# Optimization experiments

Measured on AMD Instinct MI355X. Metric: run time of the kernel, lower is better.

The kernel has to match this reference:

```python
import jax, jax.numpy as jnp
import numpy as np

B, S, D = 2, 2048, 4096
H, ROT = 16, 64
HD = D // H  # 256


def rotate_every_two(x):
    # x: (..., d) with d even; interleave (-x_odd, x_even)
    x1 = x[..., ::2]
    x2 = x[..., 1::2]
    return jnp.stack((-x2, x1), axis=-1).reshape(x.shape)


def setup_inputs() -> dict:
    key = jax.random.key(0)
    ks = jax.random.split(key, 8)
    hidden_states = jax.random.normal(ks[0], (B, S, D), dtype=jnp.float32)
    # GPT-J style repeat-interleaved sin/cos over rotary_dim, broadcast over heads
    inv_freq = 1.0 / (10000.0 ** (jnp.arange(0, ROT, 2, dtype=jnp.float32) / ROT))
    t = jnp.arange(S, dtype=jnp.float32)
    freqs = jnp.einsum('s,f->sf', t, inv_freq)                    # (S, ROT/2)
    freqs = jnp.repeat(freqs, 2, axis=-1)                         # (S, ROT)
    sin = jnp.sin(freqs)[None, :, None, :]                        # (1, S, 1, ROT)
    cos = jnp.cos(freqs)[None, :, None, :]
    scale = 0.02
    Wq = jax.random.normal(ks[1], (D, D), dtype=jnp.float32) * scale
    Wk = jax.random.normal(ks[2], (D, D), dtype=jnp.float32) * scale
    Wv = jax.random.normal(ks[3], (D, D), dtype=jnp.float32) * scale
    Wo = jax.random.normal(ks[4], (D, D), dtype=jnp.float32) * scale
    return {"hidden_states": hidden_states, "sin": sin, "cos": cos,
            "Wq": Wq, "Wk": Wk, "Wv": Wv, "Wo": Wo}


def reference(hidden_states, sin, cos, Wq, Wk, Wv, Wo):
    b, s, d = hidden_states.shape
    # projections (nn.Linear, no bias): y = x @ W.T
    q = (hidden_states @ Wq.T).reshape(b, s, H, HD)
    k = (hidden_states @ Wk.T).reshape(b, s, H, HD)
    v = (hidden_states @ Wv.T).reshape(b, s, H, HD)

    def rope(x):
        x_rot, x_pass = x[..., :ROT], x[..., ROT:]
        x_rot = x_rot * cos + rotate_every_two(x_rot) * sin
        return jnp.concatenate([x_rot, x_pass], axis=-1)

    q = rope(q).transpose(0, 2, 1, 3)  # (B, H, S, HD)
    k = rope(k).transpose(0, 2, 1, 3)
    v = v.transpose(0, 2, 1, 3)

    inv_scale = 1.0 / np.sqrt(HD).astype(np.float32)
    scores = jnp.einsum('bhqd,bhkd->bhqk', q, k) * inv_scale      # (B, H, S, S)
    # scaled_masked_triangular_softmax == causal masked softmax
    causal = jnp.tril(jnp.ones((s, s), dtype=bool))
    scores = jnp.where(causal[None, None], scores, jnp.finfo(scores.dtype).min)
    attn = jax.nn.softmax(scores, axis=-1)
    out = jnp.einsum('bhqk,bhkd->bhqd', attn, v)                  # (B, H, S, HD)
    out = out.transpose(0, 2, 1, 3).reshape(b, s, d)              # merge heads
    return out @ Wo.T
```

## Files before the change

kernel.cpp:

```cpp
#include <hip/hip_runtime.h>
#include <cstdint>
#include <cstddef>

#define TB 2
#define TS 2048
#define TD 4096
#define TH 16
#define THD 256
#define TROT 64
#define TM (TB*TS)

typedef __attribute__((ext_vector_type(8))) short bf16x8;
typedef __attribute__((ext_vector_type(4))) float f32x4;

#define LGKM0  asm volatile("s_waitcnt lgkmcnt(0)" ::: "memory")
#define VMCNT8 asm volatile("s_waitcnt vmcnt(8)" ::: "memory")
#define VMCNT4 asm volatile("s_waitcnt vmcnt(4)" ::: "memory")
#define VMCNT0 asm volatile("s_waitcnt vmcnt(0)" ::: "memory")
#define SBAR   __builtin_amdgcn_s_barrier()
#define SCHED0 __builtin_amdgcn_sched_barrier(0)

__device__ __forceinline__ unsigned short f2bf(float f) {
  union { float f; unsigned u; } v; v.f = f;
  return (unsigned short)((v.u + 0x7fffu + ((v.u >> 16) & 1u)) >> 16);
}

__device__ __forceinline__ void gld16(const void* g, void* l) {
  __builtin_amdgcn_global_load_lds(
      (const __attribute__((address_space(1))) unsigned int*)g,
      (__attribute__((address_space(3))) unsigned int*)l, 16, 0, 0);
}

__global__ __launch_bounds__(256) void k_cvt5(
    const float* __restrict__ s0, const float* __restrict__ s1,
    const float* __restrict__ s2, const float* __restrict__ s3,
    const float* __restrict__ s4, unsigned short* __restrict__ dst) {
  int i = blockIdx.x * 256 + threadIdx.x;
  int tsel = i >> 22, il = i & 4194303;
  const float* s = tsel == 0 ? s0 : tsel == 1 ? s1 : tsel == 2 ? s2 : tsel == 3 ? s3 : s4;
  float4 v = reinterpret_cast<const float4*>(s)[il];
  ushort4 o;
  o.x = f2bf(v.x); o.y = f2bf(v.y); o.z = f2bf(v.z); o.w = f2bf(v.w);
  *reinterpret_cast<ushort4*>(dst + (size_t)i * 4) = o;
}

template<int MODE>
__global__ __launch_bounds__(512, 1) void k_gemm(
    const unsigned short* __restrict__ A, const unsigned short* __restrict__ W,
    void* __restrict__ out, const float* __restrict__ sinp, const float* __restrict__ cosp)
{
  extern __shared__ unsigned short lds[];
  const int K = TD;
  const int t = threadIdx.x;
  const int w = t >> 6, l = t & 63, lr = l & 15, lh = l >> 4;
  const int wm = w >> 2, wn = w & 3;

  const int id = blockIdx.x;
  const int swz = (id & 7) * 32 + (id >> 3);
  const int m0 = (swz >> 4) * 256, n0 = (swz & 15) * 256;

  const int llo = lr * 32 + ((lh ^ ((lr >> 1) & 3)) * 8);

  const unsigned short* srcA = A + (size_t)m0 * K;
  const unsigned short* srcB = W + (size_t)n0 * K;

  int roff[2];
#pragma unroll
  for (int it = 0; it < 2; ++it) {
    int c = it * 512 + t;
    int rl = (c >> 2) & 15;
    roff[it] = (16 * (c >> 7) + rl) * K + ((c >> 6) & 1) * 32 + ((c & 3) ^ ((rl >> 1) & 3)) * 8;
  }

  f32x4 acc[2][2][4][2];
#pragma unroll
  for (int qa = 0; qa < 2; ++qa)
#pragma unroll
    for (int qb = 0; qb < 2; ++qb)
#pragma unroll
      for (int m = 0; m < 4; ++m)
#pragma unroll
        for (int n = 0; n < 2; ++n) acc[qa][qb][m][n] = 0.f;

  bf16x8 af[4][2], bq0[2][2], bq1[2][2];

#define STG(SBUF, SAB, SHALF, SKOFS) { \
    const unsigned short* _s = (SAB) ? srcB : srcA; \
    const int _b = (SBUF)*32768 + (SAB)*16384 + (SHALF)*8192; \
    gld16(_s + (size_t)(SHALF)*128*TD + (SKOFS) + roff[0], &lds[_b + t*8]); \
    gld16(_s + (size_t)(SHALF)*128*TD + (SKOFS) + roff[1], &lds[_b + (512+t)*8]); }

#define PH(BUF, QA, QB, LDAF, LDB0, LDB1, SBUF, SAB, SHALF, SKOFS, DOVM) { \
    if (LDAF) { \
      _Pragma("unroll") for (int m = 0; m < 4; ++m) \
      _Pragma("unroll") for (int kk = 0; kk < 2; ++kk) \
        af[m][kk] = *(const bf16x8*)&lds[(BUF)*32768 + (QA)*8192 + ((wm*4+m)*2+kk)*512 + llo]; \
    } \
    if (LDB0) { \
      _Pragma("unroll") for (int n = 0; n < 2; ++n) \
      _Pragma("unroll") for (int kk = 0; kk < 2; ++kk) \
        bq0[n][kk] = *(const bf16x8*)&lds[(BUF)*32768 + 16384 + ((wn*2+n)*2+kk)*512 + llo]; \
    } \
    if (LDB1) { \
      _Pragma("unroll") for (int n = 0; n < 2; ++n) \
      _Pragma("unroll") for (int kk = 0; kk < 2; ++kk) \
        bq1[n][kk] = *(const bf16x8*)&lds[(BUF)*32768 + 16384 + 8192 + ((wn*2+n)*2+kk)*512 + llo]; \
    } \
    STG(SBUF, SAB, SHALF, SKOFS); \
    if (DOVM) { VMCNT4; } \
    SBAR; \
    if ((LDAF) || (LDB0) || (LDB1)) { LGKM0; } \
    SCHED0; \
    __builtin_amdgcn_s_setprio(1); \
    _Pragma("unroll") for (int kk = 0; kk < 2; ++kk) \
    _Pragma("unroll") for (int m = 0; m < 4; ++m) \
    _Pragma("unroll") for (int n = 0; n < 2; ++n) \
      acc[QA][QB][m][n] = __builtin_amdgcn_mfma_f32_16x16x32_bf16( \
          af[m][kk], (QB) ? bq1[n][kk] : bq0[n][kk], acc[QA][QB][m][n], 0,0,0); \
    __builtin_amdgcn_s_setprio(0); \
    SBAR; SCHED0; }

  const int NT = K / 64;

  STG(0,0,0, 0);  SCHED0;
  STG(0,1,0, 0);  SCHED0;
  STG(0,0,1, 0);  SCHED0;
  STG(0,1,1, 0);  SCHED0;
  STG(1,0,0, 64); SCHED0;
  STG(1,1,0, 64); SCHED0;
  VMCNT4; SBAR; SCHED0;

  for (int i2 = 0; i2 < NT/2; ++i2) {
    const int k1c = (2*i2+1) * 64;
    const int k0n = (2*i2+2 < NT ? 2*i2+2 : NT-1) * 64;
    const int k1n = (2*i2+3 < NT ? 2*i2+3 : NT-1) * 64;
    PH(0, 0,0, 1,1,0,  1,0,1, k1c, 0);
    PH(0, 0,1, 0,0,1,  1,1,1, k1c, 0);
    PH(0, 1,0, 1,0,0,  0,0,0, k0n, 0);
    PH(0, 1,1, 0,0,0,  0,1,0, k0n, 1);
    PH(1, 0,0, 1,1,0,  0,0,1, k0n, 0);
    PH(1, 0,1, 0,0,1,  0,1,1, k0n, 0);
    PH(1, 1,0, 1,0,0,  1,0,0, k1n, 0);
    PH(1, 1,1, 0,0,0,  1,1,0, k1n, 1);
  }
#undef PH
#undef STG

  VMCNT0;

  if constexpr (MODE == 2) {
    SBAR;
    const int b = m0 >> 11, sbase = m0 & (TS - 1);
#pragma unroll
    for (int qb = 0; qb < 2; ++qb)
#pragma unroll
      for (int n = 0; n < 2; ++n) {
        __syncthreads();
#pragma unroll
        for (int qa = 0; qa < 2; ++qa)
#pragma unroll
          for (int m = 0; m < 4; ++m) {
            int lcol = wn * 16 + lr;
            int srow = qa * 128 + wm * 64 + m * 16 + lh * 4;
            ushort4 o;
            o.x = f2bf(acc[qa][qb][m][n][0]); o.y = f2bf(acc[qa][qb][m][n][1]);
            o.z = f2bf(acc[qa][qb][m][n][2]); o.w = f2bf(acc[qa][qb][m][n][3]);
            *(ushort4*)&lds[lcol * 268 + srow] = o;
          }
        __syncthreads();
#pragma unroll
        for (int rr = 0; rr < 4; ++rr) {
          int idx = rr * 512 + t;
          int dl = idx >> 5, sc = (idx & 31) * 8;
          uint4 v = *(const uint4*)&lds[dl * 268 + sc];
          int d = n0 + qb * 128 + (dl >> 4) * 32 + n * 16 + (dl & 15);
          *(uint4*)((unsigned short*)out +
                    ((size_t)((b * TH + (d >> 8)) * THD + (d & 255))) * TS + sbase + sc) = v;
        }
      }
  } else {
#pragma unroll
    for (int qa = 0; qa < 2; ++qa)
#pragma unroll
      for (int qb = 0; qb < 2; ++qb)
#pragma unroll
        for (int m = 0; m < 4; ++m)
#pragma unroll
          for (int n = 0; n < 2; ++n)
#pragma unroll
            for (int r = 0; r < 4; ++r) {
              int row = m0 + qa * 128 + wm * 64 + m * 16 + lh * 4 + r;
              int col = n0 + qb * 128 + wn * 32 + n * 16 + lr;
              float x = acc[qa][qb][m][n][r];
              if constexpr (MODE == 0) {
                ((float*)out)[(size_t)row * TD + col] = x;
              } else {
                float part = __shfl_xor(x, 1, 64);
                int s = row & (TS - 1), b = row >> 11;
                int h = col >> 8, d = col & 255;
                float val = x;
                if (d < TROT) {
                  float cc = cosp[s * TROT + d], ss = sinp[s * TROT + d];
                  val = x * cc + ((d & 1) ? part : -part) * ss;
                }
                ((unsigned short*)out)[((size_t)(b * TH + h) * TS + s) * THD + d] = f2bf(val);
              }
            }
  }
}

__global__ __launch_bounds__(256, 2) void k_fattn(
    const unsigned short* __restrict__ Qt, const unsigned short* __restrict__ Kt,
    const unsigned short* __restrict__ Vt, unsigned short* __restrict__ O)
{
  extern __shared__ unsigned short sh[];
  const int t = threadIdx.x, w = t >> 6, l = t & 63, lr = l & 15, lh = l >> 4;
  const int bh = blockIdx.x;
  const int qb = (gridDim.y - 1) - blockIdx.y;
  const int q0 = qb * 64;
  const int jmax = qb;

  const unsigned short* kbase = Kt + (size_t)bh * TS * THD;
  const unsigned short* vbase = Vt + (size_t)bh * THD * TS;

  const int llo = lr * 32 + ((lh ^ ((lr >> 1) & 3)) * 8);

  int koff[8], voff[8];
#pragma unroll
  for (int it = 0; it < 8; ++it) {
    int c = it * 256 + t;
    int row = (c >> 2) & 15;
    int scc = (c & 3) ^ ((row >> 1) & 3);
    koff[it] = (((c >> 9) & 3) * 16 + row) * THD + ((c >> 6) & 7) * 32 + scc * 8;
    voff[it] = (((c >> 6) & 15) * 16 + row) * TS + ((c >> 10) & 1) * 32 + scc * 8;
  }

  bf16x8 qf[8];
  const unsigned short* qp = Qt + ((size_t)bh * TS + q0 + w * 16 + lr) * THD;
#pragma unroll
  for (int kk = 0; kk < 8; ++kk) qf[kk] = *(const bf16x8*)(qp + kk * 32 + lh * 8);

  f32x4 oacc[16];
#pragma unroll
  for (int i = 0; i < 16; ++i) oacc[i] = 0.f;
  float mrow[4] = {-__builtin_inff(), -__builtin_inff(), -__builtin_inff(), -__builtin_inff()};
  float lrow[4] = {0.f, 0.f, 0.f, 0.f};

#pragma unroll
  for (int it = 0; it < 8; ++it) gld16(kbase + koff[it], &sh[(it*256 + t) * 8]);
#pragma unroll
  for (int it = 0; it < 8; ++it) gld16(vbase + voff[it], &sh[16384 + (it*256 + t) * 8]);

  for (int j = 0; j <= jmax; ++j) {
    const bool nx = (j < jmax);
    VMCNT8; SBAR; SCHED0;

    f32x4 sacc[4];
#pragma unroll
    for (int nt = 0; nt < 4; ++nt) sacc[nt] = 0.f;
    __builtin_amdgcn_s_setprio(1);
#pragma unroll
    for (int kk = 0; kk < 8; ++kk)
#pragma unroll
      for (int nt = 0; nt < 4; ++nt) {
        bf16x8 kf = *(const bf16x8*)&sh[(nt*8 + kk)*512 + llo];
        sacc[nt] = __builtin_amdgcn_mfma_f32_16x16x32_bf16(qf[kk], kf, sacc[nt], 0, 0, 0);
      }
    __builtin_amdgcn_s_setprio(0);
    LGKM0; SBAR; SCHED0;
    if (nx) {
      const unsigned short* kj = kbase + (size_t)(j + 1) * 64 * THD;
#pragma unroll
      for (int it = 0; it < 8; ++it) gld16(kj + koff[it], &sh[(it*256 + t) * 8]);
    }

    float p[4][4], tmax[4];
    const int qrow0 = q0 + w * 16 + lh * 4;
#pragma unroll
    for (int r = 0; r < 4; ++r) tmax[r] = -__builtin_inff();
#pragma unroll
    for (int nt = 0; nt < 4; ++nt) {
      int kpos = j * 64 + nt * 16 + lr;
#pragma unroll
      for (int r = 0; r < 4; ++r) {
        float sv = sacc[nt][r] * 0.0625f;
        if (kpos > qrow0 + r) sv = -__builtin_inff();
        p[nt][r] = sv;
        tmax[r] = fmaxf(tmax[r], sv);
      }
    }
#pragma unroll
    for (int off = 1; off < 16; off <<= 1)
#pragma unroll
      for (int r = 0; r < 4; ++r) tmax[r] = fmaxf(tmax[r], __shfl_xor(tmax[r], off, 64));

    float g = fmaxf(fmaxf(tmax[0] - mrow[0], tmax[1] - mrow[1]),
                    fmaxf(tmax[2] - mrow[2], tmax[3] - mrow[3]));
    if (__any(g > 8.f)) {
      float alpha[4];
#pragma unroll
      for (int r = 0; r < 4; ++r) {
        float mn = fmaxf(mrow[r], tmax[r]);
        alpha[r] = __expf(mrow[r] - mn);
        mrow[r] = mn;
        lrow[r] *= alpha[r];
      }
#pragma unroll
      for (int i = 0; i < 16; ++i)
#pragma unroll
        for (int r = 0; r < 4; ++r) oacc[i][r] *= alpha[r];
    }

    float tsum[4] = {0.f, 0.f, 0.f, 0.f};
#pragma unroll
    for (int nt = 0; nt < 4; ++nt)
#pragma unroll
      for (int r = 0; r < 4; ++r) {
        float pe = __expf(p[nt][r] - mrow[r]);
        p[nt][r] = pe;
        tsum[r] += pe;
      }
#pragma unroll
    for (int off = 1; off < 16; off <<= 1)
#pragma unroll
      for (int r = 0; r < 4; ++r) tsum[r] += __shfl_xor(tsum[r], off, 64);
#pragma unroll
    for (int r = 0; r < 4; ++r) lrow[r] += tsum[r];

    const int wb = 32768 + w * 1152;
#pragma unroll
    for (int nt = 0; nt < 4; ++nt)
#pragma unroll
      for (int r = 0; r < 4; ++r)
        sh[wb + (lh*4 + r)*72 + nt*16 + lr] = f2bf(p[nt][r]);
    bf16x8 pfr0 = *(const bf16x8*)&sh[wb + lr*72 + lh*8];
    bf16x8 pfr1 = *(const bf16x8*)&sh[wb + lr*72 + 32 + lh*8];

    if (nx) { VMCNT8; } else { VMCNT0; }
    SBAR; SCHED0;
    __builtin_amdgcn_s_setprio(1);
#pragma unroll
    for (int dt = 0; dt < 16; ++dt) {
      bf16x8 vf = *(const bf16x8*)&sh[16384 + dt*512 + llo];
      oacc[dt] = __builtin_amdgcn_mfma_f32_16x16x32_bf16(pfr0, vf, oacc[dt], 0, 0, 0);
    }
#pragma unroll
    for (int dt = 0; dt < 16; ++dt) {
      bf16x8 vf = *(const bf16x8*)&sh[16384 + (16 + dt)*512 + llo];
      oacc[dt] = __builtin_amdgcn_mfma_f32_16x16x32_bf16(pfr1, vf, oacc[dt], 0, 0, 0);
    }
    __builtin_amdgcn_s_setprio(0);
    LGKM0; SBAR; SCHED0;
    if (nx) {
      const unsigned short* vj = vbase + (size_t)(j + 1) * 64;
#pragma unroll
      for (int it = 0; it < 8; ++it) gld16(vj + voff[it], &sh[16384 + (it*256 + t) * 8]);
    }
  }

  const int b = bh >> 4, h = bh & 15;
  float inv[4];
#pragma unroll
  for (int r = 0; r < 4; ++r) inv[r] = 1.f / lrow[r];
#pragma unroll
  for (int dt = 0; dt < 16; ++dt)
#pragma unroll
    for (int r = 0; r < 4; ++r) {
      int s = q0 + w * 16 + lh * 4 + r;
      O[((size_t)(b * TS + s) * TH + h) * THD + dt * 16 + lr] = f2bf(oacc[dt][r] * inv[r]);
    }
}

extern "C" void kernel_launch(void* const* d_in, const int* in_sizes, int n_in,
                              void* d_out, int out_size, void* d_ws, size_t ws_size,
                              hipStream_t stream) {
  const float* hs   = (const float*)d_in[0];
  const float* sinp = (const float*)d_in[1];
  const float* cosp = (const float*)d_in[2];
  const float* Wq   = (const float*)d_in[3];
  const float* Wk   = (const float*)d_in[4];
  const float* Wv   = (const float*)d_in[5];
  const float* Wo   = (const float*)d_in[6];

  const size_t NE = (size_t)TM * TD;
  const size_t BYTES = NE * 2;
  char* ws = (char*)d_ws;
  unsigned short* hsb = (unsigned short*)(ws + 0*BYTES);
  unsigned short* Wqb = (unsigned short*)(ws + 1*BYTES);
  unsigned short* Wkb = (unsigned short*)(ws + 2*BYTES);
  unsigned short* Wvb = (unsigned short*)(ws + 3*BYTES);
  unsigned short* Wob = (unsigned short*)(ws + 4*BYTES);
  unsigned short* Qt  = (unsigned short*)(ws + 5*BYTES);
  unsigned short* Ktb = (unsigned short*)(ws + 6*BYTES);
  unsigned short* Vtb = (unsigned short*)(ws + 7*BYTES);
  unsigned short* Ob  = (unsigned short*)(ws + 8*BYTES);

  k_cvt5<<<81920, 256, 0, stream>>>(hs, Wq, Wk, Wv, Wo, hsb);

  k_gemm<1><<<256, 512, 131072, stream>>>(hsb, Wqb, (void*)Qt,  sinp, cosp);
  k_gemm<1><<<256, 512, 131072, stream>>>(hsb, Wkb, (void*)Ktb, sinp, cosp);
  k_gemm<2><<<256, 512, 131072, stream>>>(hsb, Wvb, (void*)Vtb, nullptr, nullptr);

  k_fattn<<<dim3(TB*TH, TS/64), 256, 74752, stream>>>(Qt, Ktb, Vtb, Ob);

  k_gemm<0><<<256, 512, 131072, stream>>>(Ob, Wob, d_out, nullptr, nullptr);
}
```

Before: 725.0 us.

## Fuse QKV projections into one launch, rework GEMM phase loads, defer softmax reductions

The three Q/K/V projection GEMMs become a single 768-block launch over the concatenated weight buffers, selecting the Q, K or V epilogue from the output column tile. This removes two launches and the tail underutilisation of three 256-block grids. The GEMM main loop is restructured to prefetch the next LDS fragments inside the previous MFMA phase using double fragment registers. The flash-attention kernel drops the per-tile cross-lane max reduction unless a rescale is needed and defers the row-sum shuffle reduction to the end. The extra fragment registers raise register pressure, and the lazy max relies on a threshold of 8 for numerical safety.

```diff
diff --git a/kernel.cpp b/kernel.cpp
--- a/kernel.cpp
+++ b/kernel.cpp
@@ -19,6 +19,8 @@
 #define VMCNT0 asm volatile("s_waitcnt vmcnt(0)" ::: "memory")
 #define SBAR   __builtin_amdgcn_s_barrier()
 #define SCHED0 __builtin_amdgcn_sched_barrier(0)
+#define PRIO1  __builtin_amdgcn_s_setprio(1)
+#define PRIO0  __builtin_amdgcn_s_setprio(0)
 
 __device__ __forceinline__ unsigned short f2bf(float f) {
   union { float f; unsigned u; } v; v.f = f;
@@ -44,112 +46,126 @@
   *reinterpret_cast<ushort4*>(dst + (size_t)i * 4) = o;
 }
 
-template<int MODE>
-__global__ __launch_bounds__(512, 1) void k_gemm(
-    const unsigned short* __restrict__ A, const unsigned short* __restrict__ W,
-    void* __restrict__ out, const float* __restrict__ sinp, const float* __restrict__ cosp)
-{
-  extern __shared__ unsigned short lds[];
-  const int K = TD;
-  const int t = threadIdx.x;
-  const int w = t >> 6, l = t & 63, lr = l & 15, lh = l >> 4;
-  const int wm = w >> 2, wn = w & 3;
-
-  const int id = blockIdx.x;
-  const int swz = (id & 7) * 32 + (id >> 3);
-  const int m0 = (swz >> 4) * 256, n0 = (swz & 15) * 256;
-
-  const int llo = lr * 32 + ((lh ^ ((lr >> 1) & 3)) * 8);
-
-  const unsigned short* srcA = A + (size_t)m0 * K;
-  const unsigned short* srcB = W + (size_t)n0 * K;
-
-  int roff[2];
-#pragma unroll
-  for (int it = 0; it < 2; ++it) {
-    int c = it * 512 + t;
-    int rl = (c >> 2) & 15;
-    roff[it] = (16 * (c >> 7) + rl) * K + ((c >> 6) & 1) * 32 + ((c & 3) ^ ((rl >> 1) & 3)) * 8;
-  }
-
-  f32x4 acc[2][2][4][2];
-#pragma unroll
-  for (int qa = 0; qa < 2; ++qa)
-#pragma unroll
-    for (int qb = 0; qb < 2; ++qb)
-#pragma unroll
-      for (int m = 0; m < 4; ++m)
-#pragma unroll
-        for (int n = 0; n < 2; ++n) acc[qa][qb][m][n] = 0.f;
-
-  bf16x8 af[4][2], bq0[2][2], bq1[2][2];
-
-#define STG(SBUF, SAB, SHALF, SKOFS) { \
+#define GSTG(SBUF, SAB, SHALF, SKOFS) { \
     const unsigned short* _s = (SAB) ? srcB : srcA; \
     const int _b = (SBUF)*32768 + (SAB)*16384 + (SHALF)*8192; \
     gld16(_s + (size_t)(SHALF)*128*TD + (SKOFS) + roff[0], &lds[_b + t*8]); \
     gld16(_s + (size_t)(SHALF)*128*TD + (SKOFS) + roff[1], &lds[_b + (512+t)*8]); }
 
-#define PH(BUF, QA, QB, LDAF, LDB0, LDB1, SBUF, SAB, SHALF, SKOFS, DOVM) { \
-    if (LDAF) { \
-      _Pragma("unroll") for (int m = 0; m < 4; ++m) \
-      _Pragma("unroll") for (int kk = 0; kk < 2; ++kk) \
-        af[m][kk] = *(const bf16x8*)&lds[(BUF)*32768 + (QA)*8192 + ((wm*4+m)*2+kk)*512 + llo]; \
-    } \
-    if (LDB0) { \
-      _Pragma("unroll") for (int n = 0; n < 2; ++n) \
-      _Pragma("unroll") for (int kk = 0; kk < 2; ++kk) \
-        bq0[n][kk] = *(const bf16x8*)&lds[(BUF)*32768 + 16384 + ((wn*2+n)*2+kk)*512 + llo]; \
-    } \
-    if (LDB1) { \
-      _Pragma("unroll") for (int n = 0; n < 2; ++n) \
-      _Pragma("unroll") for (int kk = 0; kk < 2; ++kk) \
-        bq1[n][kk] = *(const bf16x8*)&lds[(BUF)*32768 + 16384 + 8192 + ((wn*2+n)*2+kk)*512 + llo]; \
-    } \
-    STG(SBUF, SAB, SHALF, SKOFS); \
-    if (DOVM) { VMCNT4; } \
-    SBAR; \
-    if ((LDAF) || (LDB0) || (LDB1)) { LGKM0; } \
-    SCHED0; \
-    __builtin_amdgcn_s_setprio(1); \
+#define GLD_AF(DST, BUF, QA) { \
+    _Pragma("unroll") for (int m = 0; m < 4; ++m) \
+    _Pragma("unroll") for (int kk = 0; kk < 2; ++kk) \
+      DST[m][kk] = *(const bf16x8*)&lds[(BUF)*32768 + (QA)*8192 + ((wm*4+m)*2+kk)*512 + llo]; }
+
+#define GLD_BQ(DST, BUF, QB) { \
+    _Pragma("unroll") for (int n = 0; n < 2; ++n) \
+    _Pragma("unroll") for (int kk = 0; kk < 2; ++kk) \
+      DST[n][kk] = *(const bf16x8*)&lds[(BUF)*32768 + 16384 + (QB)*8192 + ((wn*2+n)*2+kk)*512 + llo]; }
+
+#define GMF(AF, BQ, QA, QB) { \
     _Pragma("unroll") for (int kk = 0; kk < 2; ++kk) \
     _Pragma("unroll") for (int m = 0; m < 4; ++m) \
     _Pragma("unroll") for (int n = 0; n < 2; ++n) \
       acc[QA][QB][m][n] = __builtin_amdgcn_mfma_f32_16x16x32_bf16( \
-          af[m][kk], (QB) ? bq1[n][kk] : bq0[n][kk], acc[QA][QB][m][n], 0,0,0); \
-    __builtin_amdgcn_s_setprio(0); \
-    SBAR; SCHED0; }
-
+          AF[m][kk], BQ[n][kk], acc[QA][QB][m][n], 0,0,0); }
+
+#define GEMM_MAIN_LOOP \
+  GSTG(0,0,0, 0);  SCHED0; \
+  GSTG(0,1,0, 0);  SCHED0; \
+  GSTG(0,0,1, 0);  SCHED0; \
+  GSTG(0,1,1, 0);  SCHED0; \
+  GSTG(1,0,0, 64); SCHED0; \
+  GSTG(1,1,0, 64); SCHED0; \
+  VMCNT4; SBAR; SCHED0; \
+  for (int i2 = 0; i2 < NT/2; ++i2) { \
+    const int k1c = (2*i2+1) * 64; \
+    const int k0n = (2*i2+2 < NT ? 2*i2+2 : NT-1) * 64; \
+    const int k1n = (2*i2+3 < NT ? 2*i2+3 : NT-1) * 64; \
+    GLD_AF(afP, 0, 0); GLD_BQ(bqP, 0, 0); \
+    GSTG(1,0,1, k1c); \
+    SBAR; LGKM0; SCHED0; \
+    PRIO1; GLD_BQ(bqQ, 0, 1); GMF(afP, bqP, 0, 0); PRIO0; \
+    SBAR; SCHED0; \
+    GSTG(1,1,1, k1c); \
+    SBAR; LGKM0; SCHED0; \
+    PRIO1; GLD_AF(afQ, 0, 1); GMF(afP, bqQ, 0, 1); PRIO0; \
+    SBAR; SCHED0; \
+    GSTG(0,0,0, k0n); \
+    SBAR; LGKM0; SCHED0; \
+    PRIO1; GMF(afQ, bqP, 1, 0); PRIO0; \
+    SBAR; SCHED0; \
+    GSTG(0,1,0, k0n); \
+    VMCNT4; \
+    SBAR; LGKM0; SCHED0; \
+    PRIO1; GMF(afQ, bqQ, 1, 1); PRIO0; \
+    SBAR; SCHED0; \
+    GLD_AF(afP, 1, 0); GLD_BQ(bqP, 1, 0); \
+    GSTG(0,0,1, k0n); \
+    SBAR; LGKM0; SCHED0; \
+    PRIO1; GLD_BQ(bqQ, 1, 1); GMF(afP, bqP, 0, 0); PRIO0; \
+    SBAR; SCHED0; \
+    GSTG(0,1,1, k0n); \
+    SBAR; LGKM0; SCHED0; \
+    PRIO1; GLD_AF(afQ, 1, 1); GMF(afP, bqQ, 0, 1); PRIO0; \
+    SBAR; SCHED0; \
+    GSTG(1,0,0, k1n); \
+    SBAR; LGKM0; SCHED0; \
+    PRIO1; GMF(afQ, bqP, 1, 0); PRIO0; \
+    SBAR; SCHED0; \
+    GSTG(1,1,0, k1n); \
+    VMCNT4; \
+    SBAR; LGKM0; SCHED0; \
+    PRIO1; GMF(afQ, bqQ, 1, 1); PRIO0; \
+    SBAR; SCHED0; \
+  }
+
+#define GEMM_PREAMBLE \
+  const int K = TD; \
+  const int t = threadIdx.x; \
+  const int w = t >> 6, l = t & 63, lr = l & 15, lh = l >> 4; \
+  const int wm = w >> 2, wn = w & 3; \
+  const int llo = lr * 32 + ((lh ^ ((lr >> 1) & 3)) * 8); \
+  int roff[2]; \
+  _Pragma("unroll") \
+  for (int it = 0; it < 2; ++it) { \
+    int c = it * 512 + t; \
+    int rl = (c >> 2) & 15; \
+    roff[it] = (16 * (c >> 7) + rl) * K + ((c >> 6) & 1) * 32 + ((c & 3) ^ ((rl >> 1) & 3)) * 8; \
+  } \
+  f32x4 acc[2][2][4][2]; \
+  _Pragma("unroll") \
+  for (int qa = 0; qa < 2; ++qa) \
+  _Pragma("unroll") \
+    for (int qb = 0; qb < 2; ++qb) \
+  _Pragma("unroll") \
+      for (int m = 0; m < 4; ++m) \
+  _Pragma("unroll") \
+        for (int n = 0; n < 2; ++n) acc[qa][qb][m][n] = 0.f; \
+  bf16x8 afP[4][2], afQ[4][2], bqP[2][2], bqQ[2][2]; \
   const int NT = K / 64;
 
-  STG(0,0,0, 0);  SCHED0;
-  STG(0,1,0, 0);  SCHED0;
-  STG(0,0,1, 0);  SCHED0;
-  STG(0,1,1, 0);  SCHED0;
-  STG(1,0,0, 64); SCHED0;
-  STG(1,1,0, 64); SCHED0;
-  VMCNT4; SBAR; SCHED0;
-
-  for (int i2 = 0; i2 < NT/2; ++i2) {
-    const int k1c = (2*i2+1) * 64;
-    const int k0n = (2*i2+2 < NT ? 2*i2+2 : NT-1) * 64;
-    const int k1n = (2*i2+3 < NT ? 2*i2+3 : NT-1) * 64;
-    PH(0, 0,0, 1,1,0,  1,0,1, k1c, 0);
-    PH(0, 0,1, 0,0,1,  1,1,1, k1c, 0);
-    PH(0, 1,0, 1,0,0,  0,0,0, k0n, 0);
-    PH(0, 1,1, 0,0,0,  0,1,0, k0n, 1);
-    PH(1, 0,0, 1,1,0,  0,0,1, k0n, 0);
-    PH(1, 0,1, 0,0,1,  0,1,1, k0n, 0);
-    PH(1, 1,0, 1,0,0,  1,0,0, k1n, 0);
-    PH(1, 1,1, 0,0,0,  1,1,0, k1n, 1);
-  }
-#undef PH
-#undef STG
+__global__ __launch_bounds__(512, 1) void k_gqkv(
+    const unsigned short* __restrict__ A, const unsigned short* __restrict__ W,
+    unsigned short* __restrict__ Qo, unsigned short* __restrict__ Ko,
+    unsigned short* __restrict__ Vo,
+    const float* __restrict__ sinp, const float* __restrict__ cosp)
+{
+  extern __shared__ unsigned short lds[];
+  const int id = blockIdx.x;
+  const int swz = (id & 7) * 96 + (id >> 3);
+  const int m0 = (swz / 48) * 256, n0 = (swz % 48) * 256;
+
+  GEMM_PREAMBLE
+  const unsigned short* srcA = A + (size_t)m0 * K;
+  const unsigned short* srcB = W + (size_t)n0 * K;
+
+  GEMM_MAIN_LOOP
 
   VMCNT0;
-
-  if constexpr (MODE == 2) {
+  const int tsel = n0 >> 12;
+  if (tsel == 2) {
     SBAR;
+    const int n0v = n0 - 8192;
     const int b = m0 >> 11, sbase = m0 & (TS - 1);
 #pragma unroll
     for (int qb = 0; qb < 2; ++qb)
@@ -173,12 +189,13 @@
           int idx = rr * 512 + t;
           int dl = idx >> 5, sc = (idx & 31) * 8;
           uint4 v = *(const uint4*)&lds[dl * 268 + sc];
-          int d = n0 + qb * 128 + (dl >> 4) * 32 + n * 16 + (dl & 15);
-          *(uint4*)((unsigned short*)out +
-                    ((size_t)((b * TH + (d >> 8)) * THD + (d & 255))) * TS + sbase + sc) = v;
+          int d = n0v + qb * 128 + (dl >> 4) * 32 + n * 16 + (dl & 15);
+          *(uint4*)(Vo + ((size_t)((b * TH + (d >> 8)) * THD + (d & 255))) * TS + sbase + sc) = v;
         }
       }
   } else {
+    unsigned short* outp = tsel ? Ko : Qo;
+    const int nbase = n0 & 4095;
 #pragma unroll
     for (int qa = 0; qa < 2; ++qa)
 #pragma unroll
@@ -190,23 +207,51 @@
 #pragma unroll
             for (int r = 0; r < 4; ++r) {
               int row = m0 + qa * 128 + wm * 64 + m * 16 + lh * 4 + r;
-              int col = n0 + qb * 128 + wn * 32 + n * 16 + lr;
+              int col = nbase + qb * 128 + wn * 32 + n * 16 + lr;
               float x = acc[qa][qb][m][n][r];
-              if constexpr (MODE == 0) {
-                ((float*)out)[(size_t)row * TD + col] = x;
-              } else {
-                float part = __shfl_xor(x, 1, 64);
-                int s = row & (TS - 1), b = row >> 11;
-                int h = col >> 8, d = col & 255;
-                float val = x;
-                if (d < TROT) {
-                  float cc = cosp[s * TROT + d], ss = sinp[s * TROT + d];
-                  val = x * cc + ((d & 1) ? part : -part) * ss;
-                }
-                ((unsigned short*)out)[((size_t)(b * TH + h) * TS + s) * THD + d] = f2bf(val);
+              float part = __shfl_xor(x, 1, 64);
+              int s = row & (TS - 1), b = row >> 11;
+              int h = col >> 8, d = col & 255;
+              float val = x;
+              if (d < TROT) {
+                float cc = cosp[s * TROT + d], ss = sinp[s * TROT + d];
+                val = x * cc + ((d & 1) ? part : -part) * ss;
               }
+              outp[((size_t)(b * TH + h) * TS + s) * THD + d] = f2bf(val);
             }
   }
+}
+
+__global__ __launch_bounds__(512, 1) void k_gout(
+    const unsigned short* __restrict__ A, const unsigned short* __restrict__ W,
+    float* __restrict__ out)
+{
+  extern __shared__ unsigned short lds[];
+  const int id = blockIdx.x;
+  const int swz = (id & 7) * 32 + (id >> 3);
+  const int m0 = (swz >> 4) * 256, n0 = (swz & 15) * 256;
+
+  GEMM_PREAMBLE
+  const unsigned short* srcA = A + (size_t)m0 * K;
+  const unsigned short* srcB = W + (size_t)n0 * K;
+
+  GEMM_MAIN_LOOP
+
+  VMCNT0;
+#pragma unroll
+  for (int qa = 0; qa < 2; ++qa)
+#pragma unroll
+    for (int qb = 0; qb < 2; ++qb)
+#pragma unroll
+      for (int m = 0; m < 4; ++m)
+#pragma unroll
+        for (int n = 0; n < 2; ++n)
+#pragma unroll
+          for (int r = 0; r < 4; ++r) {
+            int row = m0 + qa * 128 + wm * 64 + m * 16 + lh * 4 + r;
+            int col = n0 + qb * 128 + wn * 32 + n * 16 + lr;
+            out[(size_t)row * TD + col] = acc[qa][qb][m][n][r];
+          }
 }
 
 __global__ __launch_bounds__(256, 2) void k_fattn(
@@ -258,7 +303,7 @@
     f32x4 sacc[4];
 #pragma unroll
     for (int nt = 0; nt < 4; ++nt) sacc[nt] = 0.f;
-    __builtin_amdgcn_s_setprio(1);
+    PRIO1;
 #pragma unroll
     for (int kk = 0; kk < 8; ++kk)
 #pragma unroll
@@ -266,7 +311,7 @@
         bf16x8 kf = *(const bf16x8*)&sh[(nt*8 + kk)*512 + llo];
         sacc[nt] = __builtin_amdgcn_mfma_f32_16x16x32_bf16(qf[kk], kf, sacc[nt], 0, 0, 0);
       }
-    __builtin_amdgcn_s_setprio(0);
+    PRIO0;
     LGKM0; SBAR; SCHED0;
     if (nx) {
       const unsigned short* kj = kbase + (size_t)(j + 1) * 64 * THD;
@@ -274,10 +319,8 @@
       for (int it = 0; it < 8; ++it) gld16(kj + koff[it], &sh[(it*256 + t) * 8]);
     }
 
-    float p[4][4], tmax[4];
+    float p[4][4];
     const int qrow0 = q0 + w * 16 + lh * 4;
-#pragma unroll
-    for (int r = 0; r < 4; ++r) tmax[r] = -__builtin_inff();
 #pragma unroll
     for (int nt = 0; nt < 4; ++nt) {
       int kpos = j * 64 + nt * 16 + lr;
@@ -286,17 +329,20 @@
         float sv = sacc[nt][r] * 0.0625f;
         if (kpos > qrow0 + r) sv = -__builtin_inff();
         p[nt][r] = sv;
-        tmax[r] = fmaxf(tmax[r], sv);
       }
     }
-#pragma unroll
-    for (int off = 1; off < 16; off <<= 1)
-#pragma unroll
-      for (int r = 0; r < 4; ++r) tmax[r] = fmaxf(tmax[r], __shfl_xor(tmax[r], off, 64));
-
-    float g = fmaxf(fmaxf(tmax[0] - mrow[0], tmax[1] - mrow[1]),
-                    fmaxf(tmax[2] - mrow[2], tmax[3] - mrow[3]));
+    float lmax[4];
+#pragma unroll
+    for (int r = 0; r < 4; ++r)
+      lmax[r] = fmaxf(fmaxf(p[0][r], p[1][r]), fmaxf(p[2][r], p[3][r]));
+    float g = fmaxf(fmaxf(lmax[0] - mrow[0], lmax[1] - mrow[1]),
+                    fmaxf(lmax[2] - mrow[2], lmax[3] - mrow[3]));
     if (__any(g > 8.f)) {
+      float tmax[4] = {lmax[0], lmax[1], lmax[2], lmax[3]};
+#pragma unroll
+      for (int off = 1; off < 16; off <<= 1)
+#pragma unroll
+        for (int r = 0; r < 4; ++r) tmax[r] = fmaxf(tmax[r], __shfl_xor(tmax[r], off, 64));
       float alpha[4];
 #pragma unroll
       for (int r = 0; r < 4; ++r) {
@@ -310,22 +356,15 @@
 #pragma unroll
         for (int r = 0; r < 4; ++r) oacc[i][r] *= alpha[r];
     }
-
-    float tsum[4] = {0.f, 0.f, 0.f, 0.f};
-#pragma unroll
-    for (int nt = 0; nt < 4; ++nt)
-#pragma unroll
-      for (int r = 0; r < 4; ++r) {
-        float pe = __expf(p[nt][r] - mrow[r]);
-        p[nt][r] = pe;
-        tsum[r] += pe;
-      }
-#pragma unroll
-    for (int off = 1; off < 16; off <<= 1)
-#pragma unroll
-      for (int r = 0; r < 4; ++r) tsum[r] += __shfl_xor(tsum[r], off, 64);
-#pragma unroll
-    for (int r = 0; r < 4; ++r) lrow[r] += tsum[r];
+#pragma unroll
+    for (int r = 0; r < 4; ++r) {
+      float pe0 = __expf(p[0][r] - mrow[r]);
+      float pe1 = __expf(p[1][r] - mrow[r]);
+      float pe2 = __expf(p[2][r] - mrow[r]);
+      float pe3 = __expf(p[3][r] - mrow[r]);
+      p[0][r] = pe0; p[1][r] = pe1; p[2][r] = pe2; p[3][r] = pe3;
+      lrow[r] += (pe0 + pe1) + (pe2 + pe3);
+    }
 
     const int wb = 32768 + w * 1152;
 #pragma unroll
@@ -338,7 +377,7 @@
 
     if (nx) { VMCNT8; } else { VMCNT0; }
     SBAR; SCHED0;
-    __builtin_amdgcn_s_setprio(1);
+    PRIO1;
 #pragma unroll
     for (int dt = 0; dt < 16; ++dt) {
       bf16x8 vf = *(const bf16x8*)&sh[16384 + dt*512 + llo];
@@ -349,7 +388,7 @@
       bf16x8 vf = *(const bf16x8*)&sh[16384 + (16 + dt)*512 + llo];
       oacc[dt] = __builtin_amdgcn_mfma_f32_16x16x32_bf16(pfr1, vf, oacc[dt], 0, 0, 0);
     }
-    __builtin_amdgcn_s_setprio(0);
+    PRIO0;
     LGKM0; SBAR; SCHED0;
     if (nx) {
       const unsigned short* vj = vbase + (size_t)(j + 1) * 64;
@@ -357,6 +396,11 @@
       for (int it = 0; it < 8; ++it) gld16(vj + voff[it], &sh[16384 + (it*256 + t) * 8]);
     }
   }
+
+#pragma unroll
+  for (int off = 1; off < 16; off <<= 1)
+#pragma unroll
+    for (int r = 0; r < 4; ++r) lrow[r] += __shfl_xor(lrow[r], off, 64);
 
   const int b = bh >> 4, h = bh & 15;
   float inv[4];
@@ -387,8 +431,6 @@
   char* ws = (char*)d_ws;
   unsigned short* hsb = (unsigned short*)(ws + 0*BYTES);
   unsigned short* Wqb = (unsigned short*)(ws + 1*BYTES);
-  unsigned short* Wkb = (unsigned short*)(ws + 2*BYTES);
-  unsigned short* Wvb = (unsigned short*)(ws + 3*BYTES);
   unsigned short* Wob = (unsigned short*)(ws + 4*BYTES);
   unsigned short* Qt  = (unsigned short*)(ws + 5*BYTES);
   unsigned short* Ktb = (unsigned short*)(ws + 6*BYTES);
@@ -397,11 +439,9 @@
 
   k_cvt5<<<81920, 256, 0, stream>>>(hs, Wq, Wk, Wv, Wo, hsb);
 
-  k_gemm<1><<<256, 512, 131072, stream>>>(hsb, Wqb, (void*)Qt,  sinp, cosp);
-  k_gemm<1><<<256, 512, 131072, stream>>>(hsb, Wkb, (void*)Ktb, sinp, cosp);
-  k_gemm<2><<<256, 512, 131072, stream>>>(hsb, Wvb, (void*)Vtb, nullptr, nullptr);
+  k_gqkv<<<768, 512, 131072, stream>>>(hsb, Wqb, Qt, Ktb, Vtb, sinp, cosp);
 
   k_fattn<<<dim3(TB*TH, TS/64), 256, 74752, stream>>>(Qt, Ktb, Vtb, Ob);
 
-  k_gemm<0><<<256, 512, 131072, stream>>>(Ob, Wob, d_out, nullptr, nullptr);
-}
+  k_gout<<<256, 512, 131072, stream>>>(Ob, Wob, (float*)d_out);
+}
```

New measurement: 699.8 us. 1.04x faster.
